# Optimization experiments

Hardware: AMD Instinct MI355X
Metric: run time of the kernel (lower is better)

The kernel has to match this reference:

```python
import jax, jax.numpy as jnp
import numpy as np

# dims (Nemotron-H 8B class mamba mixer)
HID = 4096      # hidden_size
NH = 128        # mamba_num_heads
HD = 64         # mamba_head_dim
DIN = NH * HD   # intermediate_size = 8192
G = 8           # n_groups
N = 128         # ssm_state_size
K = 4           # conv_kernel
CS = 256        # chunk_size
EPS = 1e-5
GROUP_SIZE = DIN // G
CONV_DIM = DIN + 2 * G * N           # 10240
PROJ = DIN + CONV_DIM + NH           # 18560 = gate | xBC | dt


def segment_sum(x):
    """x: [..., k] -> [..., k, k]; out[i,j] = sum_{m=j+1..i} x[m], -inf above diag."""
    k = x.shape[-1]
    xe = jnp.broadcast_to(x[..., None], x.shape + (k,))
    xe = jnp.where(jnp.tril(jnp.ones((k, k), bool), -1), xe, 0.0)
    s = jnp.cumsum(xe, axis=-2)
    return jnp.where(jnp.tril(jnp.ones((k, k), bool), 0), s, -jnp.inf)


def setup_inputs() -> dict:
    key = jax.random.key(0)
    ks = jax.random.split(key, 9)
    std = 0.02
    return {
        "hidden_states": jax.random.normal(ks[0], (2, 2048, HID), jnp.float32),
        "in_proj_w": jax.random.normal(ks[1], (PROJ, HID), jnp.float32) * std,
        "conv_w": jax.random.normal(ks[2], (CONV_DIM, 1, K), jnp.float32) * 0.1,
        "conv_b": jax.random.normal(ks[3], (CONV_DIM,), jnp.float32) * 0.01,
        "dt_bias": jax.random.uniform(ks[4], (NH,), jnp.float32, -4.0, -2.0),
        "A_log": jnp.log(jax.random.uniform(ks[5], (NH,), jnp.float32, 1.0, 16.0)),
        "D": jnp.ones((NH,), jnp.float32),
        "norm_w": jnp.ones((DIN,), jnp.float32),
        "out_proj_w": jax.random.normal(ks[8], (HID, DIN), jnp.float32) * std,
    }


def reference(hidden_states, in_proj_w, conv_w, conv_b, dt_bias, A_log, D, norm_w, out_proj_w):
    b, l, _ = hidden_states.shape
    zxbcdt = hidden_states @ in_proj_w.T                       # [b,l,PROJ]
    gate = zxbcdt[..., :DIN]
    xBC = zxbcdt[..., DIN:DIN + CONV_DIM]
    dt = zxbcdt[..., DIN + CONV_DIM:]                          # [b,l,NH]

    # causal depthwise conv1d + silu
    conv = jax.lax.conv_general_dilated(
        jnp.transpose(xBC, (0, 2, 1)), conv_w, (1,), [(K - 1, 0)],
        feature_group_count=CONV_DIM, dimension_numbers=("NCH", "OIH", "NCH"))
    xBC = jax.nn.silu(jnp.transpose(conv + conv_b[None, :, None], (0, 2, 1)))

    x = xBC[..., :DIN].reshape(b, l, NH, HD)
    B = xBC[..., DIN:DIN + G * N].reshape(b, l, G, N)
    C = xBC[..., DIN + G * N:].reshape(b, l, G, N)
    B = jnp.repeat(B, NH // G, axis=2)                         # [b,l,NH,N]
    C = jnp.repeat(C, NH // G, axis=2)

    A = -jnp.exp(A_log)                                        # [NH]
    dt = jax.nn.softplus(dt + dt_bias)                         # [b,l,NH]; limit (0,inf) is a no-op

    pad = (CS - l % CS) % CS
    def padl(t):
        return jnp.pad(t, [(0, 0), (0, pad)] + [(0, 0)] * (t.ndim - 2))

    D_res = D[None, None, :, None] * padl(x)                   # [b,L,NH,HD]
    xs = x * dt[..., None]
    Adt = A[None, None, :] * dt                                # [b,l,NH]

    nc = (l + pad) // CS
    def chunk(t):
        return padl(t).reshape((b, nc, CS) + t.shape[2:])
    xs, B, C = chunk(xs), chunk(B), chunk(C)                   # [b,c,k,h,*]
    Ac = jnp.transpose(chunk(Adt), (0, 3, 1, 2))               # [b,h,c,k]
    A_cumsum = jnp.cumsum(Ac, axis=-1)

    # 1. intra-chunk (diagonal blocks)
    L = jnp.exp(segment_sum(Ac))                               # [b,h,c,k,k]
    Gm = jnp.einsum("bcihn,bcjhn->bhcij", C, B)
    Y_diag = jnp.einsum("bhcij,bcjhd->bcihd", Gm * L, xs)

    # 2. chunk states
    decay_states = jnp.exp(A_cumsum[..., -1:] - A_cumsum)      # [b,h,c,k]
    states = jnp.einsum("bckhn,bhck,bckhd->bchdn", B, decay_states, xs)

    # 3. inter-chunk recurrence
    A_tail = jnp.pad(A_cumsum[..., -1], ((0, 0), (0, 0), (1, 0)))
    decay_chunk = jnp.exp(segment_sum(A_tail))                 # [b,h,c+1,c+1]
    states = jnp.concatenate([jnp.zeros_like(states[:, :1]), states], axis=1)
    new_states = jnp.einsum("bhzc,bchdn->bzhdn", decay_chunk, states)
    states = new_states[:, :-1]                                # [b,c,h,d,n]

    # 4. state -> output
    state_decay = jnp.exp(A_cumsum)                            # [b,h,c,k]
    Y_off = jnp.einsum("bckhn,bchdn,bhck->bckhd", C, states, state_decay)

    y = (Y_diag + Y_off).reshape(b, l + pad, NH, HD) + D_res
    y = y[:, :l].reshape(b, l, DIN)

    # gated grouped RMSNorm
    y = y * jax.nn.silu(gate)
    yg = y.reshape(b, l, G, GROUP_SIZE)
    var = jnp.mean(yg * yg, axis=-1, keepdims=True)
    y = (yg * jax.lax.rsqrt(var + EPS)).reshape(b, l, DIN) * norm_w
    return y @ out_proj_w.T
```

## Files before the change

### kernel.cpp

```cpp
#include <hip/hip_runtime.h>
#include <hip/hip_bf16.h>
#include <math.h>

#define HID 4096
#define NH 128
#define HD 64
#define DIN 8192
#define G 8
#define NSTATE 128
#define CS 256
#define GROUP_SIZE 1024
#define CONV_DIM 10240
#define ZXW 18432
#define BATCH 2
#define SEQ 2048
#define NT (BATCH*SEQ)
#define NC 8
#define DTSK 16

typedef __attribute__((ext_vector_type(8))) short bf16x8;
typedef __attribute__((ext_vector_type(4))) float f32x4;
typedef __attribute__((ext_vector_type(8))) unsigned short u16x8;
typedef __attribute__((ext_vector_type(4))) unsigned short u16x4;

__device__ __forceinline__ float sigmoidf_(float x){ return 1.f/(1.f+expf(-x)); }
__device__ __forceinline__ float siluf_(float x){ return x*sigmoidf_(x); }
__device__ __forceinline__ float softplusf_(float x){ return (x>20.f)? x : log1pf(expf(x)); }
__device__ __forceinline__ float b2f(unsigned short u){ union{unsigned int i; float f;} x; x.i = ((unsigned int)u)<<16; return x.f; }
__device__ __forceinline__ unsigned short f2b(float f){ __hip_bfloat16 h = __float2bfloat16(f); return *(unsigned short*)&h; }

__device__ __forceinline__ void gload_lds16(const void* g, void* l) {
  __builtin_amdgcn_global_load_lds((const __attribute__((address_space(1))) unsigned int*)g,
                                   (__attribute__((address_space(3))) unsigned int*)l, 16, 0, 0);
}
__device__ __forceinline__ bf16x8 ld8bf(const __hip_bfloat16* p){ return *(const bf16x8*)p; }

__device__ __forceinline__ void cast8(const float* in, __hip_bfloat16* out) {
  const float4* p = (const float4*)in;
  float4 a = p[0], b = p[1];
  union { __hip_bfloat16 h[8]; int4 v; } o;
  o.h[0]=__float2bfloat16(a.x); o.h[1]=__float2bfloat16(a.y);
  o.h[2]=__float2bfloat16(a.z); o.h[3]=__float2bfloat16(a.w);
  o.h[4]=__float2bfloat16(b.x); o.h[5]=__float2bfloat16(b.y);
  o.h[6]=__float2bfloat16(b.z); o.h[7]=__float2bfloat16(b.w);
  *(int4*)out = o.v;
}

__global__ __launch_bounds__(256)
void cast3_kernel(const float* __restrict__ hs, __hip_bfloat16* __restrict__ hs_bf,
                  const float* __restrict__ w_in, __hip_bfloat16* __restrict__ w_in_bf,
                  const float* __restrict__ w_out, __hip_bfloat16* __restrict__ w_out_bf) {
  const size_t n0 = (size_t)NT*HID/8;
  const size_t n1 = (size_t)ZXW*HID/8;
  const size_t n2 = (size_t)HID*DIN/8;
  const size_t ntot = n0 + n1 + n2;
  size_t i = (size_t)blockIdx.x * 256 + threadIdx.x;
  size_t stride = (size_t)gridDim.x * 256;
  for (; i < ntot; i += stride) {
    if (i < n0)            cast8(hs   + i*8,        hs_bf   + i*8);
    else if (i < n0 + n1)  cast8(w_in + (i-n0)*8,   w_in_bf + (i-n0)*8);
    else                   cast8(w_out+ (i-n0-n1)*8, w_out_bf+ (i-n0-n1)*8);
  }
}

template<bool OUT_BF16>
__global__ __launch_bounds__(512)
void gemm_bf16_256(const __hip_bfloat16* __restrict__ A, const __hip_bfloat16* __restrict__ B,
                   void* __restrict__ Cout, int M, int N, int K) {
  const int nMt = M >> 8, nNt = N >> 8;
  const int nwg = nMt * nNt;
  const int cpx = nwg >> 3;
  const int lin = blockIdx.x;
  const int swz = (lin & 7) * cpx + (lin >> 3);
  const int mt = swz % nMt, ntile = swz / nMt;
  const int rowBase = mt << 8;
  const int colBase = ntile << 8;

  __shared__ short As[4][8192];
  __shared__ short Bs[4][8192];

  const int tid = threadIdx.x;
  const int lane = tid & 63, wid = tid >> 6;
  const int wr = wid >> 2, wc = wid & 3;
  const int l15 = lane & 15, l4 = lane >> 4;

  const int r0 = tid >> 2,        c0 = (tid & 3) ^ ((r0 >> 1) & 3);
  const int r1 = (512+tid) >> 2,  c1 = ((512+tid) & 3) ^ ((r1 >> 1) & 3);
  const __hip_bfloat16* gA0 = A + (size_t)(rowBase + r0)*K + c0*8;
  const __hip_bfloat16* gA1 = A + (size_t)(rowBase + r1)*K + c1*8;
  const __hip_bfloat16* gB0 = B + (size_t)(colBase + r0)*K + c0*8;
  const __hip_bfloat16* gB1 = B + (size_t)(colBase + r1)*K + c1*8;
  const int ld0 = wid*512, ld1 = 4096 + wid*512;

#define STAGE_A(q, kt) do { \
    gload_lds16(gA0 + (size_t)(kt)*32, (void*)&As[q][ld0]); \
    gload_lds16(gA1 + (size_t)(kt)*32, (void*)&As[q][ld1]); \
  } while(0)
#define STAGE_B(q, kt) do { \
    gload_lds16(gB0 + (size_t)(kt)*32, (void*)&Bs[q][ld0]); \
    gload_lds16(gB1 + (size_t)(kt)*32, (void*)&Bs[q][ld1]); \
  } while(0)

  int aoff[8], boff[4];
  #pragma unroll
  for (int m=0;m<8;++m){ int r = wr*128 + m*16 + l15; aoff[m] = r*32 + ((l4 ^ ((r>>1)&3))*8); }
  #pragma unroll
  for (int n=0;n<4;++n){ int r = wc*64  + n*16 + l15; boff[n] = r*32 + ((l4 ^ ((r>>1)&3))*8); }

  f32x4 acc[8][4] = {};
  const int NKT = K >> 5;

  STAGE_A(0,0); STAGE_B(0,0);
  STAGE_A(1,1); STAGE_B(1,1);
  STAGE_A(2,2); STAGE_B(2,2);
  asm volatile("s_waitcnt vmcnt(8)" ::: "memory");
  __builtin_amdgcn_s_barrier();

  for (int t = 0; t < NKT; ++t) {
    const short* ab = &As[t&3][0];
    const short* bb = &Bs[t&3][0];
    const int q3 = (t+3)&3;
    bf16x8 a[4], b[4], a2[4];
    #pragma unroll
    for (int m=0;m<4;++m) a[m] = *(const bf16x8*)&ab[aoff[m]];
    #pragma unroll
    for (int n=0;n<4;++n) b[n] = *(const bf16x8*)&bb[boff[n]];
    if (t + 3 < NKT) STAGE_A(q3, t+3);
    __builtin_amdgcn_s_barrier();
    asm volatile("s_waitcnt lgkmcnt(0)" ::: "memory");
    __builtin_amdgcn_sched_barrier(0);
    __builtin_amdgcn_s_setprio(1);
    #pragma unroll
    for (int m=0;m<4;++m)
      #pragma unroll
      for (int n=0;n<4;++n)
        acc[m][n] = __builtin_amdgcn_mfma_f32_16x16x32_bf16(a[m], b[n], acc[m][n], 0, 0, 0);
    __builtin_amdgcn_s_setprio(0);
    __builtin_amdgcn_s_barrier();
    #pragma unroll
    for (int m=0;m<4;++m) a2[m] = *(const bf16x8*)&ab[aoff[m+4]];
    if (t + 3 < NKT) STAGE_B(q3, t+3);
    const int rem = NKT - 1 - t;
    if (rem >= 3)      asm volatile("s_waitcnt vmcnt(8)" ::: "memory");
    else if (rem == 2) asm volatile("s_waitcnt vmcnt(4)" ::: "memory");
    else if (rem == 1) asm volatile("s_waitcnt vmcnt(0)" ::: "memory");
    __builtin_amdgcn_s_barrier();
    asm volatile("s_waitcnt lgkmcnt(0)" ::: "memory");
    __builtin_amdgcn_sched_barrier(0);
    __builtin_amdgcn_s_setprio(1);
    #pragma unroll
    for (int m=0;m<4;++m)
      #pragma unroll
      for (int n=0;n<4;++n)
        acc[m+4][n] = __builtin_amdgcn_mfma_f32_16x16x32_bf16(a2[m], b[n], acc[m+4][n], 0, 0, 0);
    __builtin_amdgcn_s_setprio(0);
    __builtin_amdgcn_s_barrier();
  }
#undef STAGE_A
#undef STAGE_B

  #pragma unroll
  for (int m=0;m<8;++m) {
    int row0 = rowBase + wr*128 + m*16 + l4*4;
    #pragma unroll
    for (int n=0;n<4;++n) {
      int col = colBase + wc*64 + n*16 + l15;
      #pragma unroll
      for (int j=0;j<4;++j) {
        if (OUT_BF16)
          ((__hip_bfloat16*)Cout)[(size_t)(row0+j)*N + col] = __float2bfloat16(acc[m][n][j]);
        else
          ((float*)Cout)[(size_t)(row0+j)*N + col] = acc[m][n][j];
      }
    }
  }
}

__global__ __launch_bounds__(256)
void dt_gemm_splitk(const float* __restrict__ A, const float* __restrict__ B,
                    float* __restrict__ partial) {
  __shared__ float As[16][132];
  __shared__ float Bs[16][132];
  const int tid = threadIdx.x;
  const int tx = tid & 15, ty = tid >> 4;
  const int rowBase = blockIdx.y * 128;
  const int k0 = blockIdx.x * (HID/DTSK);
  float acc[8][8] = {};
  for (int kt = k0; kt < k0 + HID/DTSK; kt += 16) {
    for (int e = tid; e < 128*16; e += 256) {
      int r = e >> 4, c = e & 15;
      As[c][r] = A[(size_t)(rowBase + r) * HID + kt + c];
      Bs[c][r] = B[(size_t)r * HID + kt + c];
    }
    __syncthreads();
    #pragma unroll
    for (int kk = 0; kk < 16; ++kk) {
      float a[8], bv[8];
      #pragma unroll
      for (int i = 0; i < 8; ++i) a[i] = As[kk][ty*8+i];
      #pragma unroll
      for (int j = 0; j < 8; ++j) bv[j] = Bs[kk][tx*8+j];
      #pragma unroll
      for (int i = 0; i < 8; ++i)
        #pragma unroll
        for (int j = 0; j < 8; ++j)
          acc[i][j] += a[i]*bv[j];
    }
    __syncthreads();
  }
  float* outp = partial + (size_t)blockIdx.x * NT * NH;
  for (int i = 0; i < 8; ++i) {
    size_t ro = (size_t)(rowBase + ty*8 + i) * NH + tx*8;
    #pragma unroll
    for (int j = 0; j < 8; ++j) outp[ro + j] = acc[i][j];
  }
}

__global__ __launch_bounds__(256)
void dt_reduce_kernel(const float* __restrict__ partial, float* __restrict__ dtb) {
  int idx = blockIdx.x*256 + threadIdx.x;
  float s = 0.f;
  #pragma unroll
  for (int sk = 0; sk < DTSK; ++sk) s += partial[(size_t)sk*NT*NH + idx];
  dtb[idx] = s;
}

__global__ __launch_bounds__(256)
void conv_silu_kernel(const __hip_bfloat16* __restrict__ zx, const float* __restrict__ w,
                      const float* __restrict__ bias,
                      __hip_bfloat16* __restrict__ xbf,
                      __hip_bfloat16* __restrict__ Bbf,
                      __hip_bfloat16* __restrict__ Cbf) {
  int idx = blockIdx.x * 256 + threadIdx.x;
  int c8 = idx % (CONV_DIM/8);
  int t  = idx / (CONV_DIM/8);
  int c0 = c8 * 8;
  int l = t & (SEQ-1);
  float acc[8];
  *(float4*)&acc[0] = *(const float4*)&bias[c0];
  *(float4*)&acc[4] = *(const float4*)&bias[c0+4];
  float4 wv[8];
  #pragma unroll
  for (int q=0;q<8;++q) wv[q] = *(const float4*)&w[(c0+q)*4];
  #pragma unroll
  for (int k=0;k<4;++k) {
    if (l - 3 + k >= 0) {
      u16x8 v = *(const u16x8*)&zx[(size_t)(t-3+k)*ZXW + DIN + c0];
      #pragma unroll
      for (int q=0;q<8;++q) acc[q] += b2f(v[q]) * ((const float*)&wv[q])[k];
    }
  }
  u16x8 o;
  #pragma unroll
  for (int q=0;q<8;++q) o[q] = f2b(siluf_(acc[q]));
  if (c0 < DIN) *(u16x8*)&xbf[(size_t)t*DIN + c0] = o;
  else if (c0 < DIN + G*NSTATE) *(u16x8*)&Bbf[(size_t)t*(G*NSTATE) + (c0 - DIN)] = o;
  else *(u16x8*)&Cbf[(size_t)t*(G*NSTATE) + (c0 - DIN - G*NSTATE)] = o;
}

__global__ __launch_bounds__(256)
void dt_scan_kernel(float* __restrict__ dtbuf, const float* __restrict__ dt_bias,
                    const float* __restrict__ A_log, float* __restrict__ Acs) {
  int bid = blockIdx.x;
  int c = bid % NC;
  int h = (bid / NC) % NH;
  int b = bid / (NC*NH);
  int k = threadIdx.x;
  int t = b*SEQ + c*CS + k;
  float raw = dtbuf[(size_t)t*NH + h] + dt_bias[h];
  float dtv = softplusf_(raw);
  dtbuf[(size_t)t*NH + h] = dtv;
  float adt = -expf(A_log[h]) * dtv;
  __shared__ float s[CS];
  s[k] = adt;
  __syncthreads();
  for (int off = 1; off < CS; off <<= 1) {
    float v = (k >= off) ? s[k-off] : 0.f;
    __syncthreads();
    s[k] += v;
    __syncthreads();
  }
  Acs[((size_t)(b*NH + h)*NC + c)*CS + k] = s[k];
}

__global__ __launch_bounds__(256)
void prep_xt_kernel(const __hip_bfloat16* __restrict__ xbf, const float* __restrict__ dt_sp,
                    const float* __restrict__ Acs,
                    __hip_bfloat16* __restrict__ xsT, __hip_bfloat16* __restrict__ xwT) {
  int tt = blockIdx.x;
  int h  = blockIdx.y;
  int t0 = tt*64;
  int b = t0 >> 11, cc = (t0 >> 8) & 7, k0 = t0 & 255;
  __shared__ unsigned short T[64][72];
  __shared__ float dts[64], ews[64];
  int tid = threadIdx.x;
  if (tid < 64) {
    int t = t0 + tid;
    dts[tid] = dt_sp[(size_t)t*NH + h];
    const float* acs = Acs + ((size_t)(b*NH+h)*NC + cc)*CS;
    ews[tid] = __expf(acs[CS-1] - acs[k0 + tid]);
  }
  #pragma unroll
  for (int it = 0; it < 2; ++it) {
    int r = tid >> 2;
    int c8 = (tid & 3) + it*4;
    u16x8 v = *(const u16x8*)&xbf[(size_t)(t0+r)*DIN + h*64 + c8*8];
    #pragma unroll
    for (int q=0;q<8;++q) T[c8*8+q][r] = v[q];
  }
  __syncthreads();
  #pragma unroll
  for (int it = 0; it < 2; ++it) {
    int ch = tid >> 2;
    int tc = (tid & 3) + it*4;
    u16x8 v = *(const u16x8*)&T[ch][tc*8];
    u16x8 a, wv;
    #pragma unroll
    for (int q=0;q<8;++q) {
      float f = b2f(v[q]);
      float fs = f * dts[tc*8+q];
      a[q]  = f2b(fs);
      wv[q] = f2b(fs * ews[tc*8+q]);
    }
    *(u16x8*)&xsT[(size_t)(h*64+ch)*NT + t0 + tc*8] = a;
    *(u16x8*)&xwT[(size_t)(h*64+ch)*NT + t0 + tc*8] = wv;
  }
}

__global__ __launch_bounds__(256)
void transpose_bf16_kernel(const __hip_bfloat16* __restrict__ src, __hip_bfloat16* __restrict__ dst, int S) {
  int tt = blockIdx.x;
  int ct = blockIdx.y;
  int t0 = tt*64, c0 = ct*64;
  __shared__ unsigned short T[64][72];
  int tid = threadIdx.x;
  #pragma unroll
  for (int it = 0; it < 2; ++it) {
    int r = tid >> 2;
    int c8 = (tid & 3) + it*4;
    u16x8 v = *(const u16x8*)&src[(size_t)(t0+r)*S + c0 + c8*8];
    #pragma unroll
    for (int q=0;q<8;++q) T[c8*8+q][r] = v[q];
  }
  __syncthreads();
  #pragma unroll
  for (int it = 0; it < 2; ++it) {
    int ch = tid >> 2;
    int tc = (tid & 3) + it*4;
    u16x8 v = *(const u16x8*)&T[ch][tc*8];
    *(u16x8*)&dst[(size_t)(c0+ch)*NT + t0 + tc*8] = v;
  }
}

__global__ __launch_bounds__(256)
void chunk_states_mfma(const __hip_bfloat16* __restrict__ xwT, const __hip_bfloat16* __restrict__ BT,
                       float* __restrict__ states) {
  int h = blockIdx.x, bc = blockIdx.y;
  int g = h >> 4;
  int b = bc >> 3, c = bc & 7;
  int tbase = b*SEQ + c*CS;
  int tid = threadIdx.x, lane = tid & 63, w = tid >> 6;
  int l15 = lane & 15, l4 = lane >> 4;
  int n0 = w*32;
  const __hip_bfloat16* xp = xwT + (size_t)(h*64 + l15)*NT + tbase + l4*8;
  const __hip_bfloat16* bp = BT + (size_t)(g*128 + n0 + l15)*NT + tbase + l4*8;
  f32x4 acc[4][2] = {};
  for (int kc = 0; kc < 8; ++kc) {
    bf16x8 xf[4], bf2[2];
    #pragma unroll
    for (int tm=0;tm<4;++tm) xf[tm] = ld8bf(xp + (size_t)(tm*16)*NT + kc*32);
    #pragma unroll
    for (int tn=0;tn<2;++tn) bf2[tn] = ld8bf(bp + (size_t)(tn*16)*NT + kc*32);
    #pragma unroll
    for (int tm=0;tm<4;++tm)
      #pragma unroll
      for (int tn=0;tn<2;++tn)
        acc[tm][tn] = __builtin_amdgcn_mfma_f32_16x16x32_bf16(xf[tm], bf2[tn], acc[tm][tn], 0, 0, 0);
  }
  float* out = states + ((size_t)bc*NH + h)*(HD*NSTATE);
  #pragma unroll
  for (int tm=0;tm<4;++tm)
    #pragma unroll
    for (int tn=0;tn<2;++tn)
      #pragma unroll
      for (int q=0;q<4;++q)
        out[(size_t)(tm*16 + l4*4 + q)*NSTATE + n0 + tn*16 + l15] = acc[tm][tn][q];
}

__global__ void state_recurrence_kernel(const float* __restrict__ states, const float* __restrict__ Acs,
                                        __hip_bfloat16* __restrict__ states_bf) {
  int idx = blockIdx.x*256 + threadIdx.x;
  int dn = idx & 8191;
  int h = (idx >> 13) & 127;
  int b = idx >> 20;
  float S = 0.f;
  for (int c = 0; c < NC; ++c) {
    size_t off = ((size_t)(b*NC + c)*NH + h)*8192 + dn;
    float v = states[off];
    states_bf[off] = __float2bfloat16(S);
    float decay = expf(Acs[((size_t)(b*NH+h)*NC + c)*CS + CS-1]);
    S = S*decay + v;
  }
}

__global__ __launch_bounds__(256)
void y_mfma_kernel(const __hip_bfloat16* __restrict__ zx,
                   const __hip_bfloat16* __restrict__ Cn,
                   const __hip_bfloat16* __restrict__ Bn,
                   const __hip_bfloat16* __restrict__ xsT,
                   const __hip_bfloat16* __restrict__ Sbf,
                   const float* __restrict__ dt_sp,
                   const float* __restrict__ Acs,
                   const float* __restrict__ Dp,
                   __hip_bfloat16* __restrict__ ybf) {
  int h = blockIdx.x;
  int bc = blockIdx.y;
  int c = bc & 7, b = bc >> 3;
  int g = h >> 4;
  int tbase = b*SEQ + c*CS;
  int tid = threadIdx.x, lane = tid & 63, w = tid >> 6;
  int l15 = lane & 15, l4 = lane >> 4;
  int i0 = w*64;
  __shared__ float acs_s[CS];
  __shared__ unsigned short P[4][64][72];
  acs_s[tid] = Acs[((size_t)(b*NH+h)*NC + c)*CS + tid];
  __syncthreads();

  float acs_i[4], rd[4];
  float Dh = Dp[h];
  #pragma unroll
  for (int ti=0;ti<4;++ti) {
    int ig = i0 + ti*16 + l15;
    acs_i[ti] = acs_s[ig];
    rd[ti] = Dh / dt_sp[(size_t)(tbase+ig)*NH + h];
  }
  const __hip_bfloat16* Cbase = Cn + (size_t)tbase*1024 + g*128;
  const __hip_bfloat16* Bbase = Bn + (size_t)tbase*1024 + g*128;
  const __hip_bfloat16* xbase = xsT + (size_t)(h*64 + l15)*NT + tbase;

  f32x4 accY[4][4] = {};
  for (int jb = 0; jb <= w; ++jb) {
    int j0 = jb*64;
    f32x4 sacc[4][4] = {};
    for (int kc = 0; kc < 4; ++kc) {
      bf16x8 bfr[4], cfr[4];
      #pragma unroll
      for (int tj=0;tj<4;++tj) bfr[tj] = ld8bf(Bbase + (size_t)(j0 + tj*16 + l15)*1024 + kc*32 + l4*8);
      #pragma unroll
      for (int ti=0;ti<4;++ti) cfr[ti] = ld8bf(Cbase + (size_t)(i0 + ti*16 + l15)*1024 + kc*32 + l4*8);
      #pragma unroll
      for (int tj=0;tj<4;++tj)
        #pragma unroll
        for (int ti=0;ti<4;++ti)
          sacc[tj][ti] = __builtin_amdgcn_mfma_f32_16x16x32_bf16(bfr[tj], cfr[ti], sacc[tj][ti], 0, 0, 0);
    }
    #pragma unroll
    for (int tj=0;tj<4;++tj)
      #pragma unroll
      for (int ti=0;ti<4;++ti) {
        int ig = i0 + ti*16 + l15;
        float ai = acs_i[ti];
        u16x4 pk;
        #pragma unroll
        for (int q=0;q<4;++q) {
          int jg = j0 + tj*16 + l4*4 + q;
          float v = (jg <= ig) ? sacc[tj][ti][q] * __expf(ai - acs_s[jg]) : 0.f;
          if (jg == ig) v += rd[ti];
          pk[q] = f2b(v);
        }
        *(u16x4*)&P[w][ti*16 + l15][tj*16 + l4*4] = pk;
      }
    #pragma unroll
    for (int kc2 = 0; kc2 < 2; ++kc2) {
      bf16x8 xf[4], pf[4];
      #pragma unroll
      for (int tm=0;tm<4;++tm) xf[tm] = ld8bf(xbase + (size_t)(tm*16)*NT + j0 + kc2*32 + l4*8);
      #pragma unroll
      for (int ti=0;ti<4;++ti) pf[ti] = *(const bf16x8*)&P[w][ti*16 + l15][kc2*32 + l4*8];
      #pragma unroll
      for (int tm=0;tm<4;++tm)
        #pragma unroll
        for (int ti=0;ti<4;++ti)
          accY[tm][ti] = __builtin_amdgcn_mfma_f32_16x16x32_bf16(xf[tm], pf[ti], accY[tm][ti], 0, 0, 0);
    }
  }
  const __hip_bfloat16* Sb = Sbf + ((size_t)bc*NH + h)*(HD*NSTATE);
  f32x4 oacc[4][4] = {};
  for (int kc = 0; kc < 4; ++kc) {
    bf16x8 sf[4], cfr[4];
    #pragma unroll
    for (int tm=0;tm<4;++tm) sf[tm] = ld8bf(Sb + (size_t)(tm*16 + l15)*NSTATE + kc*32 + l4*8);
    #pragma unroll
    for (int ti=0;ti<4;++ti) cfr[ti] = ld8bf(Cbase + (size_t)(i0 + ti*16 + l15)*1024 + kc*32 + l4*8);
    #pragma unroll
    for (int tm=0;tm<4;++tm)
      #pragma unroll
      for (int ti=0;ti<4;++ti)
        oacc[tm][ti] = __builtin_amdgcn_mfma_f32_16x16x32_bf16(sf[tm], cfr[ti], oacc[tm][ti], 0, 0, 0);
  }
  #pragma unroll
  for (int ti=0;ti<4;++ti) {
    int ig = i0 + ti*16 + l15;
    int t = tbase + ig;
    float sd = __expf(acs_i[ti]);
    #pragma unroll
    for (int tm=0;tm<4;++tm) {
      int ch0 = h*64 + tm*16 + l4*4;
      u16x4 gv = *(const u16x4*)&zx[(size_t)t*ZXW + ch0];
      u16x4 out;
      #pragma unroll
      for (int q=0;q<4;++q) {
        float yv = accY[tm][ti][q] + sd * oacc[tm][ti][q];
        yv *= siluf_(b2f(gv[q]));
        out[q] = f2b(yv);
      }
      *(u16x4*)&ybf[(size_t)t*DIN + ch0] = out;
    }
  }
}

__global__ __launch_bounds__(256)
void groupnorm_bf16_kernel(unsigned short* __restrict__ y, const float* __restrict__ norm_w) {
  int bid = blockIdx.x;
  int g = bid % G;
  int t = bid / G;
  unsigned short* yp = y + (size_t)t*DIN + g*GROUP_SIZE;
  int tid = threadIdx.x;
  u16x4 v = *(const u16x4*)&yp[tid*4];
  float f[4]; float ss = 0.f;
  #pragma unroll
  for (int j=0;j<4;++j) { f[j] = b2f(v[j]); ss += f[j]*f[j]; }
  #pragma unroll
  for (int off = 32; off > 0; off >>= 1) ss += __shfl_xor(ss, off);
  __shared__ float wsum[4];
  int wave = tid >> 6;
  if ((tid & 63) == 0) wsum[wave] = ss;
  __syncthreads();
  float tot = wsum[0]+wsum[1]+wsum[2]+wsum[3];
  float rs = rsqrtf(tot/(float)GROUP_SIZE + 1e-5f);
  const float* nw = norm_w + g*GROUP_SIZE + tid*4;
  u16x4 o;
  #pragma unroll
  for (int j=0;j<4;++j) o[j] = f2b(f[j] * rs * nw[j]);
  *(u16x4*)&yp[tid*4] = o;
}

extern "C" void kernel_launch(void* const* d_in, const int* in_sizes, int n_in,
                              void* d_out, int out_size, void* d_ws, size_t ws_size,
                              hipStream_t stream) {
  const float* hs        = (const float*)d_in[0];
  const float* in_proj_w = (const float*)d_in[1];
  const float* conv_w    = (const float*)d_in[2];
  const float* conv_b    = (const float*)d_in[3];
  const float* dt_bias   = (const float*)d_in[4];
  const float* A_log     = (const float*)d_in[5];
  const float* Dp        = (const float*)d_in[6];
  const float* norm_w    = (const float*)d_in[7];
  const float* out_proj_w= (const float*)d_in[8];
  float* outp = (float*)d_out;

  char* ws = (char*)d_ws;
  __hip_bfloat16* zx_bf = (__hip_bfloat16*)ws;
  char* p = ws + (size_t)NT*ZXW*2;
  __hip_bfloat16* x_bf  = (__hip_bfloat16*)p; p += (size_t)NT*DIN*2;
  __hip_bfloat16* B_bf  = (__hip_bfloat16*)p; p += (size_t)NT*G*NSTATE*2;
  __hip_bfloat16* C_bf  = (__hip_bfloat16*)p; p += (size_t)NT*G*NSTATE*2;
  __hip_bfloat16* BT    = (__hip_bfloat16*)p; p += (size_t)NT*G*NSTATE*2;
  float* states = (float*)p;  p += (size_t)BATCH*NC*NH*HD*NSTATE*4;
  __hip_bfloat16* y_bf  = (__hip_bfloat16*)p; p += (size_t)NT*DIN*2;
  float* dtb    = (float*)p;  p += (size_t)NT*NH*4;
  float* Acs    = (float*)p;  p += (size_t)BATCH*NH*NC*CS*4;
  float* dt_part = (float*)y_bf;
  char* F = p;
  __hip_bfloat16* w_in_bf   = (__hip_bfloat16*)F;
  __hip_bfloat16* xsT       = (__hip_bfloat16*)F;
  __hip_bfloat16* xwT       = (__hip_bfloat16*)(F + 67108864);
  __hip_bfloat16* hs_bf     = (__hip_bfloat16*)(F + 150994944);
  __hip_bfloat16* states_bf = (__hip_bfloat16*)(F + 150994944);
  char* F2 = F + 150994944 + 33554432;
  __hip_bfloat16* w_out_bf  = (__hip_bfloat16*)F2;

  dt_gemm_splitk<<<dim3(DTSK, NT/128), 256, 0, stream>>>(hs, in_proj_w + (size_t)ZXW*HID, dt_part);
  dt_reduce_kernel<<<(NT*NH)/256, 256, 0, stream>>>(dt_part, dtb);

  cast3_kernel<<<4096, 256, 0, stream>>>(hs, hs_bf, in_proj_w, w_in_bf, out_proj_w, w_out_bf);

  gemm_bf16_256<true><<<dim3((NT/256)*(ZXW/256)), 512, 0, stream>>>(
      hs_bf, w_in_bf, zx_bf, NT, ZXW, HID);

  conv_silu_kernel<<<(NT*CONV_DIM/8)/256, 256, 0, stream>>>(zx_bf, conv_w, conv_b, x_bf, B_bf, C_bf);
  dt_scan_kernel<<<BATCH*NH*NC, CS, 0, stream>>>(dtb, dt_bias, A_log, Acs);
  prep_xt_kernel<<<dim3(NT/64, NH), 256, 0, stream>>>(x_bf, dtb, Acs, xsT, xwT);
  transpose_bf16_kernel<<<dim3(NT/64, (G*NSTATE)/64), 256, 0, stream>>>(B_bf, BT, G*NSTATE);
  chunk_states_mfma<<<dim3(NH, BATCH*NC), 256, 0, stream>>>(xwT, BT, states);
  state_recurrence_kernel<<<(BATCH*NH*HD*NSTATE)/256, 256, 0, stream>>>(states, Acs, states_bf);
  y_mfma_kernel<<<dim3(NH, BATCH*NC), 256, 0, stream>>>(zx_bf, C_bf, B_bf, xsT, states_bf, dtb, Acs, Dp, y_bf);
  groupnorm_bf16_kernel<<<NT*G, 256, 0, stream>>>((unsigned short*)y_bf, norm_w);

  gemm_bf16_256<false><<<dim3((NT/256)*(HID/256)), 512, 0, stream>>>(
      y_bf, w_out_bf, outp, NT, HID, DIN);
}
```

Baseline: 1.889 ms.

## Restructure bf16 GEMM to double-buffered 64-wide K tiles

Replaces the 4-stage, 32-wide K pipeline with a 2-stage double buffer over 64-wide K tiles. Each tile is loaded in one batch of direct-to-LDS loads with an 8-way XOR swizzle, and the fine-grained vmcnt/barrier choreography is replaced by one wait and one barrier per iteration. The aim is fewer barriers and less per-iteration synchronisation overhead with more MFMA work per tile. In exchange prefetch depth drops to one tile, so global-load latency may be less well hidden, and register pressure rises because eight A fragments are held at once.

```diff
diff --git a/kernel.cpp b/kernel.cpp
--- a/kernel.cpp
+++ b/kernel.cpp
@@ -76,88 +76,74 @@
   const int rowBase = mt << 8;
   const int colBase = ntile << 8;
 
-  __shared__ short As[4][8192];
-  __shared__ short Bs[4][8192];
+  __shared__ short As[2][16384];
+  __shared__ short Bs[2][16384];
 
   const int tid = threadIdx.x;
   const int lane = tid & 63, wid = tid >> 6;
   const int wr = wid >> 2, wc = wid & 3;
   const int l15 = lane & 15, l4 = lane >> 4;
 
-  const int r0 = tid >> 2,        c0 = (tid & 3) ^ ((r0 >> 1) & 3);
-  const int r1 = (512+tid) >> 2,  c1 = ((512+tid) & 3) ^ ((r1 >> 1) & 3);
-  const __hip_bfloat16* gA0 = A + (size_t)(rowBase + r0)*K + c0*8;
-  const __hip_bfloat16* gA1 = A + (size_t)(rowBase + r1)*K + c1*8;
-  const __hip_bfloat16* gB0 = B + (size_t)(colBase + r0)*K + c0*8;
-  const __hip_bfloat16* gB1 = B + (size_t)(colBase + r1)*K + c1*8;
-  const int ld0 = wid*512, ld1 = 4096 + wid*512;
-
-#define STAGE_A(q, kt) do { \
-    gload_lds16(gA0 + (size_t)(kt)*32, (void*)&As[q][ld0]); \
-    gload_lds16(gA1 + (size_t)(kt)*32, (void*)&As[q][ld1]); \
+  const int rB = tid >> 3;
+  const int cg = (tid & 7) ^ (rB & 7);
+  const size_t K64 = (size_t)64 * K;
+  const __hip_bfloat16* gA = A + (size_t)(rowBase + rB)*K + cg*8;
+  const __hip_bfloat16* gB = B + (size_t)(colBase + rB)*K + cg*8;
+  const int lb = wid * 512;
+
+#define STAGE(q, kt) do { \
+    gload_lds16(gA + (size_t)(kt)*64,          (void*)&As[q][lb]); \
+    gload_lds16(gA + (size_t)(kt)*64 + K64,    (void*)&As[q][4096 + lb]); \
+    gload_lds16(gA + (size_t)(kt)*64 + 2*K64,  (void*)&As[q][8192 + lb]); \
+    gload_lds16(gA + (size_t)(kt)*64 + 3*K64,  (void*)&As[q][12288 + lb]); \
+    gload_lds16(gB + (size_t)(kt)*64,          (void*)&Bs[q][lb]); \
+    gload_lds16(gB + (size_t)(kt)*64 + K64,    (void*)&Bs[q][4096 + lb]); \
+    gload_lds16(gB + (size_t)(kt)*64 + 2*K64,  (void*)&Bs[q][8192 + lb]); \
+    gload_lds16(gB + (size_t)(kt)*64 + 3*K64,  (void*)&Bs[q][12288 + lb]); \
   } while(0)
-#define STAGE_B(q, kt) do { \
-    gload_lds16(gB0 + (size_t)(kt)*32, (void*)&Bs[q][ld0]); \
-    gload_lds16(gB1 + (size_t)(kt)*32, (void*)&Bs[q][ld1]); \
-  } while(0)
 
   int aoff[8], boff[4];
   #pragma unroll
-  for (int m=0;m<8;++m){ int r = wr*128 + m*16 + l15; aoff[m] = r*32 + ((l4 ^ ((r>>1)&3))*8); }
-  #pragma unroll
-  for (int n=0;n<4;++n){ int r = wc*64  + n*16 + l15; boff[n] = r*32 + ((l4 ^ ((r>>1)&3))*8); }
+  for (int m=0;m<8;++m){ int r = wr*128 + m*16 + l15; aoff[m] = r*64 + ((l4 ^ (r&7))*8); }
+  #pragma unroll
+  for (int n=0;n<4;++n){ int r = wc*64  + n*16 + l15; boff[n] = r*64 + ((l4 ^ (r&7))*8); }
 
   f32x4 acc[8][4] = {};
-  const int NKT = K >> 5;
-
-  STAGE_A(0,0); STAGE_B(0,0);
-  STAGE_A(1,1); STAGE_B(1,1);
-  STAGE_A(2,2); STAGE_B(2,2);
-  asm volatile("s_waitcnt vmcnt(8)" ::: "memory");
-  __builtin_amdgcn_s_barrier();
+  const int NKT = K >> 6;
+
+  STAGE(0, 0);
 
   for (int t = 0; t < NKT; ++t) {
-    const short* ab = &As[t&3][0];
-    const short* bb = &Bs[t&3][0];
-    const int q3 = (t+3)&3;
-    bf16x8 a[4], b[4], a2[4];
-    #pragma unroll
-    for (int m=0;m<4;++m) a[m] = *(const bf16x8*)&ab[aoff[m]];
+    asm volatile("s_waitcnt vmcnt(0)" ::: "memory");
+    __builtin_amdgcn_s_barrier();
+    if (t + 1 < NKT) STAGE((t+1)&1, t+1);
+    const short* ab = &As[t&1][0];
+    const short* bb = &Bs[t&1][0];
+    bf16x8 a[8], b[4];
+    #pragma unroll
+    for (int m=0;m<8;++m) a[m] = *(const bf16x8*)&ab[aoff[m]];
     #pragma unroll
     for (int n=0;n<4;++n) b[n] = *(const bf16x8*)&bb[boff[n]];
-    if (t + 3 < NKT) STAGE_A(q3, t+3);
-    __builtin_amdgcn_s_barrier();
-    asm volatile("s_waitcnt lgkmcnt(0)" ::: "memory");
-    __builtin_amdgcn_sched_barrier(0);
     __builtin_amdgcn_s_setprio(1);
     #pragma unroll
-    for (int m=0;m<4;++m)
+    for (int m=0;m<8;++m)
       #pragma unroll
       for (int n=0;n<4;++n)
         acc[m][n] = __builtin_amdgcn_mfma_f32_16x16x32_bf16(a[m], b[n], acc[m][n], 0, 0, 0);
     __builtin_amdgcn_s_setprio(0);
-    __builtin_amdgcn_s_barrier();
-    #pragma unroll
-    for (int m=0;m<4;++m) a2[m] = *(const bf16x8*)&ab[aoff[m+4]];
-    if (t + 3 < NKT) STAGE_B(q3, t+3);
-    const int rem = NKT - 1 - t;
-    if (rem >= 3)      asm volatile("s_waitcnt vmcnt(8)" ::: "memory");
-    else if (rem == 2) asm volatile("s_waitcnt vmcnt(4)" ::: "memory");
-    else if (rem == 1) asm volatile("s_waitcnt vmcnt(0)" ::: "memory");
-    __builtin_amdgcn_s_barrier();
-    asm volatile("s_waitcnt lgkmcnt(0)" ::: "memory");
-    __builtin_amdgcn_sched_barrier(0);
+    #pragma unroll
+    for (int m=0;m<8;++m) a[m] = *(const bf16x8*)&ab[aoff[m] ^ 32];
+    #pragma unroll
+    for (int n=0;n<4;++n) b[n] = *(const bf16x8*)&bb[boff[n] ^ 32];
     __builtin_amdgcn_s_setprio(1);
     #pragma unroll
-    for (int m=0;m<4;++m)
+    for (int m=0;m<8;++m)
       #pragma unroll
       for (int n=0;n<4;++n)
-        acc[m+4][n] = __builtin_amdgcn_mfma_f32_16x16x32_bf16(a2[m], b[n], acc[m+4][n], 0, 0, 0);
+        acc[m][n] = __builtin_amdgcn_mfma_f32_16x16x32_bf16(a[m], b[n], acc[m][n], 0, 0, 0);
     __builtin_amdgcn_s_setprio(0);
-    __builtin_amdgcn_s_barrier();
-  }
-#undef STAGE_A
-#undef STAGE_B
+  }
+#undef STAGE
 
   #pragma unroll
   for (int m=0;m<8;++m) {
```

Result: slower. 1.954 ms (+3.4%).

## Fuse conv+silu with x prep and B transpose; fold dt reduce into scan

Applied to the files above, without the earlier changes.

Merges the split-K dt reduction into the dt softplus/cumsum scan kernel. Fuses the causal conv + SiLU with the per-head dt/decay scaling and transpose of x, and with the transpose of B, into one kernel tiled over (64 tokens x 64 channels). This removes the intermediate x_bf buffer and separate kernel launches, saving a write and re-read of the activations. The cost is a less coalesced strided gather in the dt scan and more divergent per-block roles.

```diff
diff --git a/kernel.cpp b/kernel.cpp
--- a/kernel.cpp
+++ b/kernel.cpp
@@ -217,59 +217,20 @@
 }
 
 __global__ __launch_bounds__(256)
-void dt_reduce_kernel(const float* __restrict__ partial, float* __restrict__ dtb) {
-  int idx = blockIdx.x*256 + threadIdx.x;
-  float s = 0.f;
-  #pragma unroll
-  for (int sk = 0; sk < DTSK; ++sk) s += partial[(size_t)sk*NT*NH + idx];
-  dtb[idx] = s;
-}
-
-__global__ __launch_bounds__(256)
-void conv_silu_kernel(const __hip_bfloat16* __restrict__ zx, const float* __restrict__ w,
-                      const float* __restrict__ bias,
-                      __hip_bfloat16* __restrict__ xbf,
-                      __hip_bfloat16* __restrict__ Bbf,
-                      __hip_bfloat16* __restrict__ Cbf) {
-  int idx = blockIdx.x * 256 + threadIdx.x;
-  int c8 = idx % (CONV_DIM/8);
-  int t  = idx / (CONV_DIM/8);
-  int c0 = c8 * 8;
-  int l = t & (SEQ-1);
-  float acc[8];
-  *(float4*)&acc[0] = *(const float4*)&bias[c0];
-  *(float4*)&acc[4] = *(const float4*)&bias[c0+4];
-  float4 wv[8];
-  #pragma unroll
-  for (int q=0;q<8;++q) wv[q] = *(const float4*)&w[(c0+q)*4];
-  #pragma unroll
-  for (int k=0;k<4;++k) {
-    if (l - 3 + k >= 0) {
-      u16x8 v = *(const u16x8*)&zx[(size_t)(t-3+k)*ZXW + DIN + c0];
-      #pragma unroll
-      for (int q=0;q<8;++q) acc[q] += b2f(v[q]) * ((const float*)&wv[q])[k];
-    }
-  }
-  u16x8 o;
-  #pragma unroll
-  for (int q=0;q<8;++q) o[q] = f2b(siluf_(acc[q]));
-  if (c0 < DIN) *(u16x8*)&xbf[(size_t)t*DIN + c0] = o;
-  else if (c0 < DIN + G*NSTATE) *(u16x8*)&Bbf[(size_t)t*(G*NSTATE) + (c0 - DIN)] = o;
-  else *(u16x8*)&Cbf[(size_t)t*(G*NSTATE) + (c0 - DIN - G*NSTATE)] = o;
-}
-
-__global__ __launch_bounds__(256)
-void dt_scan_kernel(float* __restrict__ dtbuf, const float* __restrict__ dt_bias,
-                    const float* __restrict__ A_log, float* __restrict__ Acs) {
+void dt_scan_kernel(const float* __restrict__ partial, const float* __restrict__ dt_bias,
+                    const float* __restrict__ A_log, float* __restrict__ dt_sp,
+                    float* __restrict__ Acs) {
   int bid = blockIdx.x;
   int c = bid % NC;
   int h = (bid / NC) % NH;
   int b = bid / (NC*NH);
   int k = threadIdx.x;
   int t = b*SEQ + c*CS + k;
-  float raw = dtbuf[(size_t)t*NH + h] + dt_bias[h];
+  float raw = dt_bias[h];
+  #pragma unroll
+  for (int sk = 0; sk < DTSK; ++sk) raw += partial[(size_t)sk*NT*NH + (size_t)t*NH + h];
   float dtv = softplusf_(raw);
-  dtbuf[(size_t)t*NH + h] = dtv;
+  dt_sp[(size_t)t*NH + h] = dtv;
   float adt = -expf(A_log[h]) * dtv;
   __shared__ float s[CS];
   s[k] = adt;
@@ -284,71 +245,85 @@
 }
 
 __global__ __launch_bounds__(256)
-void prep_xt_kernel(const __hip_bfloat16* __restrict__ xbf, const float* __restrict__ dt_sp,
-                    const float* __restrict__ Acs,
-                    __hip_bfloat16* __restrict__ xsT, __hip_bfloat16* __restrict__ xwT) {
-  int tt = blockIdx.x;
-  int h  = blockIdx.y;
-  int t0 = tt*64;
-  int b = t0 >> 11, cc = (t0 >> 8) & 7, k0 = t0 & 255;
+void conv_fused_kernel(const __hip_bfloat16* __restrict__ zx, const float* __restrict__ w,
+                       const float* __restrict__ bias,
+                       const float* __restrict__ dt_sp, const float* __restrict__ Acs,
+                       __hip_bfloat16* __restrict__ xsT, __hip_bfloat16* __restrict__ xwT,
+                       __hip_bfloat16* __restrict__ Bbf, __hip_bfloat16* __restrict__ Cbf,
+                       __hip_bfloat16* __restrict__ BT) {
+  const int tt = blockIdx.x;
+  const int ct = blockIdx.y;
+  const int t0 = tt*64;
+  const int ch0 = ct*64;
+  const int tid = threadIdx.x;
   __shared__ unsigned short T[64][72];
   __shared__ float dts[64], ews[64];
-  int tid = threadIdx.x;
-  if (tid < 64) {
+
+  const bool isX = (ch0 < DIN);
+  const bool isB = (ch0 >= DIN) && (ch0 < DIN + G*NSTATE);
+
+  if (isX && tid < 64) {
+    int h = ch0 >> 6;
     int t = t0 + tid;
     dts[tid] = dt_sp[(size_t)t*NH + h];
+    int b = t0 >> 11, cc = (t0 >> 8) & 7, k0 = t0 & 255;
     const float* acs = Acs + ((size_t)(b*NH+h)*NC + cc)*CS;
     ews[tid] = __expf(acs[CS-1] - acs[k0 + tid]);
   }
+
+  const int l0 = t0 & (SEQ-1);
   #pragma unroll
   for (int it = 0; it < 2; ++it) {
     int r = tid >> 2;
     int c8 = (tid & 3) + it*4;
-    u16x8 v = *(const u16x8*)&xbf[(size_t)(t0+r)*DIN + h*64 + c8*8];
-    #pragma unroll
-    for (int q=0;q<8;++q) T[c8*8+q][r] = v[q];
-  }
+    int cb = ch0 + c8*8;
+    float acc[8];
+    *(float4*)&acc[0] = *(const float4*)&bias[cb];
+    *(float4*)&acc[4] = *(const float4*)&bias[cb+4];
+    float4 wv[8];
+    #pragma unroll
+    for (int q=0;q<8;++q) wv[q] = *(const float4*)&w[(cb+q)*4];
+    #pragma unroll
+    for (int k=0;k<4;++k) {
+      if (l0 + r - 3 + k >= 0) {
+        u16x8 v = *(const u16x8*)&zx[(size_t)(t0+r-3+k)*ZXW + DIN + cb];
+        #pragma unroll
+        for (int q=0;q<8;++q) acc[q] += b2f(v[q]) * ((const float*)&wv[q])[k];
+      }
+    }
+    u16x8 o;
+    #pragma unroll
+    for (int q=0;q<8;++q) o[q] = f2b(siluf_(acc[q]));
+    if (isX || isB) {
+      #pragma unroll
+      for (int q=0;q<8;++q) T[c8*8+q][r] = o[q];
+    }
+    if (!isX) {
+      if (isB) *(u16x8*)&Bbf[(size_t)(t0+r)*(G*NSTATE) + (cb - DIN)] = o;
+      else     *(u16x8*)&Cbf[(size_t)(t0+r)*(G*NSTATE) + (cb - DIN - G*NSTATE)] = o;
+    }
+  }
+  if (!isX && !isB) return;
   __syncthreads();
   #pragma unroll
   for (int it = 0; it < 2; ++it) {
     int ch = tid >> 2;
     int tc = (tid & 3) + it*4;
     u16x8 v = *(const u16x8*)&T[ch][tc*8];
-    u16x8 a, wv;
-    #pragma unroll
-    for (int q=0;q<8;++q) {
-      float f = b2f(v[q]);
-      float fs = f * dts[tc*8+q];
-      a[q]  = f2b(fs);
-      wv[q] = f2b(fs * ews[tc*8+q]);
-    }
-    *(u16x8*)&xsT[(size_t)(h*64+ch)*NT + t0 + tc*8] = a;
-    *(u16x8*)&xwT[(size_t)(h*64+ch)*NT + t0 + tc*8] = wv;
-  }
-}
-
-__global__ __launch_bounds__(256)
-void transpose_bf16_kernel(const __hip_bfloat16* __restrict__ src, __hip_bfloat16* __restrict__ dst, int S) {
-  int tt = blockIdx.x;
-  int ct = blockIdx.y;
-  int t0 = tt*64, c0 = ct*64;
-  __shared__ unsigned short T[64][72];
-  int tid = threadIdx.x;
-  #pragma unroll
-  for (int it = 0; it < 2; ++it) {
-    int r = tid >> 2;
-    int c8 = (tid & 3) + it*4;
-    u16x8 v = *(const u16x8*)&src[(size_t)(t0+r)*S + c0 + c8*8];
-    #pragma unroll
-    for (int q=0;q<8;++q) T[c8*8+q][r] = v[q];
-  }
-  __syncthreads();
-  #pragma unroll
-  for (int it = 0; it < 2; ++it) {
-    int ch = tid >> 2;
-    int tc = (tid & 3) + it*4;
-    u16x8 v = *(const u16x8*)&T[ch][tc*8];
-    *(u16x8*)&dst[(size_t)(c0+ch)*NT + t0 + tc*8] = v;
+    if (isX) {
+      u16x8 a, wv2;
+      #pragma unroll
+      for (int q=0;q<8;++q) {
+        float f = b2f(v[q]);
+        float fs = f * dts[tc*8+q];
+        a[q]   = f2b(fs);
+        wv2[q] = f2b(fs * ews[tc*8+q]);
+      }
+      *(u16x8*)&xsT[(size_t)(ch0+ch)*NT + t0 + tc*8] = a;
+      *(u16x8*)&xwT[(size_t)(ch0+ch)*NT + t0 + tc*8] = wv2;
+    } else {
+      *(u16x8*)&BT[(size_t)(ch0 - DIN + ch)*NT + t0 + tc*8] = v;
+    }
   }
 }
 
@@ -562,7 +537,6 @@
   char* ws = (char*)d_ws;
   __hip_bfloat16* zx_bf = (__hip_bfloat16*)ws;
   char* p = ws + (size_t)NT*ZXW*2;
-  __hip_bfloat16* x_bf  = (__hip_bfloat16*)p; p += (size_t)NT*DIN*2;
   __hip_bfloat16* B_bf  = (__hip_bfloat16*)p; p += (size_t)NT*G*NSTATE*2;
   __hip_bfloat16* C_bf  = (__hip_bfloat16*)p; p += (size_t)NT*G*NSTATE*2;
   __hip_bfloat16* BT    = (__hip_bfloat16*)p; p += (size_t)NT*G*NSTATE*2;
@@ -581,17 +555,16 @@
   __hip_bfloat16* w_out_bf  = (__hip_bfloat16*)F2;
 
   dt_gemm_splitk<<<dim3(DTSK, NT/128), 256, 0, stream>>>(hs, in_proj_w + (size_t)ZXW*HID, dt_part);
-  dt_reduce_kernel<<<(NT*NH)/256, 256, 0, stream>>>(dt_part, dtb);
+  dt_scan_kernel<<<BATCH*NH*NC, CS, 0, stream>>>(dt_part, dt_bias, A_log, dtb, Acs);
 
   cast3_kernel<<<4096, 256, 0, stream>>>(hs, hs_bf, in_proj_w, w_in_bf, out_proj_w, w_out_bf);
 
   gemm_bf16_256<true><<<dim3((NT/256)*(ZXW/256)), 512, 0, stream>>>(
       hs_bf, w_in_bf, zx_bf, NT, ZXW, HID);
 
-  conv_silu_kernel<<<(NT*CONV_DIM/8)/256, 256, 0, stream>>>(zx_bf, conv_w, conv_b, x_bf, B_bf, C_bf);
-  dt_scan_kernel<<<BATCH*NH*NC, CS, 0, stream>>>(dtb, dt_bias, A_log, Acs);
-  prep_xt_kernel<<<dim3(NT/64, NH), 256, 0, stream>>>(x_bf, dtb, Acs, xsT, xwT);
-  transpose_bf16_kernel<<<dim3(NT/64, (G*NSTATE)/64), 256, 0, stream>>>(B_bf, BT, G*NSTATE);
+  conv_fused_kernel<<<dim3(NT/64, CONV_DIM/64), 256, 0, stream>>>(
+      zx_bf, conv_w, conv_b, dtb, Acs, xsT, xwT, B_bf, C_bf, BT);
+
   chunk_states_mfma<<<dim3(NH, BATCH*NC), 256, 0, stream>>>(xwT, BT, states);
   state_recurrence_kernel<<<(BATCH*NH*HD*NSTATE)/256, 256, 0, stream>>>(states, Acs, states_bf);
   y_mfma_kernel<<<dim3(NH, BATCH*NC), 256, 0, stream>>>(zx_bf, C_bf, B_bf, xsT, states_bf, dtb, Acs, Dp, y_bf);
```

After: 1.816 ms. 1.04x faster.
